# Kernel optimization log

Measured on AMD Instinct MI355X. Metric: run time of the kernel, lower is better.

## Reference

```python
import jax, jax.numpy as jnp
import numpy as np

N = 100000   # nodes
E = 1600000  # edges
R = 20       # relations
B = 8        # bases
F_IN = 32
H = 32
F_OUT = 32


def _rel_layer(x, src, dst, etypes, V, a, w_loop, bias, activation=None):
    """DGL RelGraphConv with basis decomposition, sum aggregation, self-loop, bias.

    message m_e = x[src_e] @ W_{r_e}, W_r = sum_b a[r,b] V[b]; h_v = sum_{e->v} m_e
    Since messages are linear in x, aggregate x[src] per (dst, rel) segment first,
    then apply the relation weights once per node: same math, far less traffic.
    """
    W = jnp.einsum('rb,bio->rio', a, V)                       # [R, in, out]
    seg = dst.astype(jnp.int32) * R + etypes.astype(jnp.int32)  # [E]
    agg = jax.ops.segment_sum(x[src], seg, num_segments=N * R)  # [N*R, in]
    agg = agg.reshape(N, R, -1)
    h = jnp.einsum('nri,rio->no', agg, W) + x @ w_loop + bias   # [N, out]
    if activation is not None:
        h = activation(h)
    return h


def setup_inputs() -> dict:
    key = jax.random.key(0)
    ks = jax.random.split(key, 10)
    s = 1.0 / np.sqrt(F_IN)
    return {
        'x': jax.random.normal(ks[0], (N, F_IN), dtype=jnp.float32),
        'src': jax.random.randint(ks[1], (E,), 0, N, dtype=jnp.int32),
        'dst': jax.random.randint(ks[2], (E,), 0, N, dtype=jnp.int32),
        'etypes': jax.random.randint(ks[3], (E,), 0, R, dtype=jnp.int32),
        'V1': jax.random.normal(ks[4], (B, F_IN, H), dtype=jnp.float32) * s,
        'a1': jax.random.normal(ks[5], (R, B), dtype=jnp.float32) * s,
        'loop1': jax.random.normal(ks[6], (F_IN, H), dtype=jnp.float32) * s,
        'b1': jnp.zeros((H,), dtype=jnp.float32),
        'V2': jax.random.normal(ks[7], (B, H, F_OUT), dtype=jnp.float32) * s,
        'a2': jax.random.normal(ks[8], (R, B), dtype=jnp.float32) * s,
        'loop2': jax.random.normal(ks[9], (H, F_OUT), dtype=jnp.float32) * s,
        'b2': jnp.zeros((F_OUT,), dtype=jnp.float32),
    }


def reference(x, src, dst, etypes, V1, a1, loop1, b1, V2, a2, loop2, b2):
    h = _rel_layer(x, src, dst, etypes, V1, a1, loop1, b1, activation=jax.nn.relu)
    h = _rel_layer(h, src, dst, etypes, V2, a2, loop2, b2, activation=None)
    return h
```

## Files before the change

### kernel.cpp

```cpp
#include <hip/hip_runtime.h>
#include <hip/hip_bf16.h>

#define NN 100000
#define NE 1600000
#define NR 20
#define NB 8
#define FD 32

#define EPB 8192
#define NBB ((NE + EPB - 1) / EPB)
#define NBKT ((NN + 255) / 256)

typedef short short8 __attribute__((ext_vector_type(8)));
typedef float f32x4  __attribute__((ext_vector_type(4)));

__device__ __forceinline__ unsigned short f2bf(float f) {
  union { float f; unsigned u; } c; c.f = f;
  unsigned r = c.u + 0x7FFF + ((c.u >> 16) & 1);
  return (unsigned short)(r >> 16);
}
__device__ __forceinline__ float bf2f(unsigned short u) {
  union { unsigned u; float f; } c; c.u = ((unsigned)u) << 16; return c.f;
}

__global__ void k_hist(const int* __restrict__ dst, int* __restrict__ hist) {
  int e = blockIdx.x * 256 + threadIdx.x;
  if (e < NE) atomicAdd(&hist[dst[e]], 1);
}

__global__ void k_scan1(int* __restrict__ data, int* __restrict__ aux, int n) {
  __shared__ int sd[256];
  int t = threadIdx.x, blk = blockIdx.x;
  int base = blk * 1024 + t * 4;
  int v[4];
#pragma unroll
  for (int j = 0; j < 4; ++j) v[j] = (base + j < n) ? data[base + j] : 0;
  int s = v[0] + v[1] + v[2] + v[3];
  sd[t] = s;
  __syncthreads();
  for (int off = 1; off < 256; off <<= 1) {
    int x = (t >= off) ? sd[t - off] : 0;
    __syncthreads();
    sd[t] += x;
    __syncthreads();
  }
  int run = sd[t] - s;
  if (t == 255) aux[blk] = sd[255];
#pragma unroll
  for (int j = 0; j < 4; ++j) {
    if (base + j < n) { data[base + j] = run; run += v[j]; }
  }
}

__global__ void k_scan2(int* __restrict__ aux, int n) {
  __shared__ int sd[256];
  int t = threadIdx.x;
  int loc[9];
  int s = 0;
#pragma unroll
  for (int j = 0; j < 9; ++j) {
    int idx = t * 9 + j;
    int v = (idx < n) ? aux[idx] : 0;
    loc[j] = s;
    s += v;
  }
  sd[t] = s;
  __syncthreads();
  for (int off = 1; off < 256; off <<= 1) {
    int x = (t >= off) ? sd[t - off] : 0;
    __syncthreads();
    sd[t] += x;
    __syncthreads();
  }
  int excl = sd[t] - s;
#pragma unroll
  for (int j = 0; j < 9; ++j) {
    int idx = t * 9 + j;
    if (idx < n) aux[idx] = excl + loc[j];
  }
}

__global__ void k_scan3(int* __restrict__ data, const int* __restrict__ aux, int n) {
  int i = blockIdx.x * 256 + threadIdx.x;
  if (i < n) data[i] += aux[i >> 10];
}

__global__ void k_endcap(int* __restrict__ ioffs) {
  if (threadIdx.x == 0 && blockIdx.x == 0) ioffs[NN] = NE;
}

__global__ void __launch_bounds__(256) k_bin(const int* __restrict__ src,
                                             const int* __restrict__ dst,
                                             const int* __restrict__ et,
                                             int* __restrict__ binbuf,
                                             int* __restrict__ bcnt,
                                             int* __restrict__ segoff) {
  __shared__ int sA[512], sB[512];
  int g = blockIdx.x, t = threadIdx.x;
  int e0 = g * EPB;
  int e1 = e0 + EPB; if (e1 > NE) e1 = NE;
  sA[t] = 0; sA[t + 256] = 0;
  __syncthreads();
  for (int e = e0 + t; e < e1; e += 256) atomicAdd(&sA[dst[e] >> 8], 1);
  __syncthreads();
  for (int b = t; b < NBKT; b += 256) bcnt[g * NBKT + b] = sA[b];
  int* pa = sA; int* pb = sB;
  for (int off = 1; off < 512; off <<= 1) {
    __syncthreads();
    for (int idx = t; idx < 512; idx += 256) {
      int v = pa[idx];
      if (idx >= off) v += pa[idx - off];
      pb[idx] = v;
    }
    int* tmp = pa; pa = pb; pb = tmp;
  }
  __syncthreads();
  for (int b = t; b < NBKT; b += 256) {
    int ex = b ? pa[b - 1] : 0;
    segoff[g * NBKT + b] = e0 + ex;
    pb[b] = ex;
  }
  __syncthreads();
  for (int e = e0 + t; e < e1; e += 256) {
    int d = dst[e];
    int pos = atomicAdd(&pb[d >> 8], 1);
    binbuf[e0 + pos] = (src[e] << 13) | ((d & 255) << 5) | et[e];
  }
}

__global__ void __launch_bounds__(256) k_bsort(const int* __restrict__ binbuf,
                                               const int* __restrict__ bcnt,
                                               const int* __restrict__ segoff,
                                               const int* __restrict__ ioffs,
                                               int* __restrict__ es) {
  __shared__ int cur[256];
  __shared__ int scnt[NBB], ssof[NBB];
  int b = blockIdx.x, t = threadIdx.x;
  int node = b * 256 + t;
  cur[t] = (node < NN) ? ioffs[node] : 0;
  for (int g = t; g < NBB; g += 256) {
    scnt[g] = bcnt[g * NBKT + b];
    ssof[g] = segoff[g * NBKT + b];
  }
  __syncthreads();
  int w = t >> 6, l = t & 63;
  for (int g = w; g < NBB; g += 4) {
    int c = scnt[g], so = ssof[g];
    for (int base = l; base < c; base += 64) {
      int v = binbuf[so + base];
      int j = (v >> 5) & 255;
      int pos = atomicAdd(&cur[j], 1);
      es[pos] = ((v >> 13) << 5) | (v & 31);
    }
  }
}

__global__ void k_xcast(const float* __restrict__ x, unsigned short* __restrict__ xb) {
  int t = blockIdx.x * 256 + threadIdx.x;
  if (t >= (NN * FD) / 8) return;
  const float4* xp = reinterpret_cast<const float4*>(x) + t * 2;
  float4 a = xp[0], b = xp[1];
  short8 v;
  v[0] = (short)f2bf(a.x); v[1] = (short)f2bf(a.y);
  v[2] = (short)f2bf(a.z); v[3] = (short)f2bf(a.w);
  v[4] = (short)f2bf(b.x); v[5] = (short)f2bf(b.y);
  v[6] = (short)f2bf(b.z); v[7] = (short)f2bf(b.w);
  reinterpret_cast<short8*>(xb)[t] = v;
}

__global__ void k_bfrag(const float* __restrict__ V1, const float* __restrict__ lp1,
                        const float* __restrict__ V2, const float* __restrict__ lp2,
                        unsigned short* __restrict__ Bf1, unsigned short* __restrict__ Bf2) {
  int t = blockIdx.x * 256 + threadIdx.x;
  if (t >= 2 * 9216) return;
  int layer = t / 9216;
  int idx = t - layer * 9216;
  int kstep = idx >> 10;
  int rem = idx & 1023;
  int otile = rem >> 9;
  int li = (rem >> 3) & 63;
  int j = idx & 7;
  int k = kstep * 32 + ((li >> 4) << 3) + j;
  int o = otile * 16 + (li & 15);
  const float* V = layer ? V2 : V1;
  const float* lp = layer ? lp2 : lp1;
  float val = (k < 256) ? V[k * 32 + o] : lp[(k - 256) * 32 + o];
  (layer ? Bf2 : Bf1)[idx] = f2bf(val);
}

__global__ void __launch_bounds__(256) k_edge(const unsigned short* __restrict__ xin,
                                              const int* __restrict__ ioffs,
                                              const int* __restrict__ es,
                                              const float* __restrict__ arel,
                                              unsigned short* __restrict__ zb,
                                              int n0, int n1) {
  int wid = (blockIdx.x * 256 + threadIdx.x) >> 6;
  int nw  = (gridDim.x * 256) >> 6;
  int l = threadIdx.x & 63;
  int i = l & 31, hh = l >> 5;
  const float4* aT = reinterpret_cast<const float4*>(arel);
  for (int v = n0 + wid; v < n1; v += nw) {
    int e0 = __builtin_amdgcn_readfirstlane(ioffs[v]);
    int e1 = __builtin_amdgcn_readfirstlane(ioffs[v + 1]);
    float z0 = 0.f, z1 = 0.f, z2 = 0.f, z3 = 0.f;
    int e = e0;
    for (; e + 8 <= e1; e += 8) {
      int r0 = es[e],     r1 = es[e + 1], r2 = es[e + 2], r3 = es[e + 3];
      int r4 = es[e + 4], r5 = es[e + 5], r6 = es[e + 6], r7 = es[e + 7];
      float x0 = bf2f(xin[((r0 >> 5) << 5) | i]);
      float x1 = bf2f(xin[((r1 >> 5) << 5) | i]);
      float x2 = bf2f(xin[((r2 >> 5) << 5) | i]);
      float x3 = bf2f(xin[((r3 >> 5) << 5) | i]);
      float x4 = bf2f(xin[((r4 >> 5) << 5) | i]);
      float x5 = bf2f(xin[((r5 >> 5) << 5) | i]);
      float x6 = bf2f(xin[((r6 >> 5) << 5) | i]);
      float x7 = bf2f(xin[((r7 >> 5) << 5) | i]);
      float4 a0 = aT[((r0 & 31) << 1) | hh];
      float4 a1 = aT[((r1 & 31) << 1) | hh];
      float4 a2 = aT[((r2 & 31) << 1) | hh];
      float4 a3 = aT[((r3 & 31) << 1) | hh];
      float4 a4 = aT[((r4 & 31) << 1) | hh];
      float4 a5 = aT[((r5 & 31) << 1) | hh];
      float4 a6 = aT[((r6 & 31) << 1) | hh];
      float4 a7 = aT[((r7 & 31) << 1) | hh];
      z0 += a0.x * x0; z1 += a0.y * x0; z2 += a0.z * x0; z3 += a0.w * x0;
      z0 += a1.x * x1; z1 += a1.y * x1; z2 += a1.z * x1; z3 += a1.w * x1;
      z0 += a2.x * x2; z1 += a2.y * x2; z2 += a2.z * x2; z3 += a2.w * x2;
      z0 += a3.x * x3; z1 += a3.y * x3; z2 += a3.z * x3; z3 += a3.w * x3;
      z0 += a4.x * x4; z1 += a4.y * x4; z2 += a4.z * x4; z3 += a4.w * x4;
      z0 += a5.x * x5; z1 += a5.y * x5; z2 += a5.z * x5; z3 += a5.w * x5;
      z0 += a6.x * x6; z1 += a6.y * x6; z2 += a6.z * x6; z3 += a6.w * x6;
      z0 += a7.x * x7; z1 += a7.y * x7; z2 += a7.z * x7; z3 += a7.w * x7;
    }
    for (; e + 4 <= e1; e += 4) {
      int r0 = es[e], r1 = es[e + 1], r2 = es[e + 2], r3 = es[e + 3];
      float x0 = bf2f(xin[((r0 >> 5) << 5) | i]);
      float x1 = bf2f(xin[((r1 >> 5) << 5) | i]);
      float x2 = bf2f(xin[((r2 >> 5) << 5) | i]);
      float x3 = bf2f(xin[((r3 >> 5) << 5) | i]);
      float4 a0 = aT[((r0 & 31) << 1) | hh];
      float4 a1 = aT[((r1 & 31) << 1) | hh];
      float4 a2 = aT[((r2 & 31) << 1) | hh];
      float4 a3 = aT[((r3 & 31) << 1) | hh];
      z0 += a0.x * x0; z1 += a0.y * x0; z2 += a0.z * x0; z3 += a0.w * x0;
      z0 += a1.x * x1; z1 += a1.y * x1; z2 += a1.z * x1; z3 += a1.w * x1;
      z0 += a2.x * x2; z1 += a2.y * x2; z2 += a2.z * x2; z3 += a2.w * x2;
      z0 += a3.x * x3; z1 += a3.y * x3; z2 += a3.z * x3; z3 += a3.w * x3;
    }
    for (; e < e1; ++e) {
      int rec = es[e];
      float xv = bf2f(xin[((rec >> 5) << 5) | i]);
      float4 av = aT[((rec & 31) << 1) | hh];
      z0 += av.x * xv; z1 += av.y * xv; z2 += av.z * xv; z3 += av.w * xv;
    }
    unsigned short* zp = zb + ((size_t)(v - n0) << 8) + (hh << 7) + i;
    zp[0]  = f2bf(z0);
    zp[32] = f2bf(z1);
    zp[64] = f2bf(z2);
    zp[96] = f2bf(z3);
  }
}

__global__ void __launch_bounds__(256) k_finish(const unsigned short* __restrict__ zb,
                                                const unsigned short* __restrict__ xin,
                                                const unsigned short* __restrict__ Bfrag,
                                                const float* __restrict__ bias,
                                                float* __restrict__ out_f32,
                                                unsigned short* __restrict__ out_bf16,
                                                int n0, int n1, int do_relu) {
  int lane = threadIdx.x & 63;
  int wid = (blockIdx.x * 256 + threadIdx.x) >> 6;
  int nwv = (gridDim.x * 256) >> 6;
  const short8* Bp = reinterpret_cast<const short8*>(Bfrag);
  short8 bf[9][2];
#pragma unroll
  for (int ks = 0; ks < 9; ++ks)
#pragma unroll
    for (int ot = 0; ot < 2; ++ot)
      bf[ks][ot] = Bp[((ks * 2 + ot) << 6) + lane];
  float bsv0 = bias[lane & 15];
  float bsv1 = bias[16 + (lane & 15)];
  int cnt = n1 - n0;
  int tiles = (cnt + 15) >> 4;
  int row = lane & 15;
  int kg = lane >> 4;
  for (int t = wid; t < tiles; t += nwv) {
    int nb = t << 4;
    int r = nb + row;
    int rc = (r < cnt) ? r : (cnt - 1);
    const short8* zrow = reinterpret_cast<const short8*>(zb + ((size_t)rc << 8));
    f32x4 acc0 = {0.f, 0.f, 0.f, 0.f};
    f32x4 acc1 = {0.f, 0.f, 0.f, 0.f};
#pragma unroll
    for (int ks = 0; ks < 8; ++ks) {
      short8 af = zrow[(ks << 2) + kg];
      acc0 = __builtin_amdgcn_mfma_f32_16x16x32_bf16(af, bf[ks][0], acc0, 0, 0, 0);
      acc1 = __builtin_amdgcn_mfma_f32_16x16x32_bf16(af, bf[ks][1], acc1, 0, 0, 0);
    }
    {
      short8 xs = *reinterpret_cast<const short8*>(xin + ((size_t)(n0 + rc) << 5) + (kg << 3));
      acc0 = __builtin_amdgcn_mfma_f32_16x16x32_bf16(xs, bf[8][0], acc0, 0, 0, 0);
      acc1 = __builtin_amdgcn_mfma_f32_16x16x32_bf16(xs, bf[8][1], acc1, 0, 0, 0);
    }
#pragma unroll
    for (int q = 0; q < 4; ++q) {
      int orow = (kg << 2) + q;
      int n = nb + orow;
      if (n < cnt) {
        float v0 = acc0[q] + bsv0;
        float v1 = acc1[q] + bsv1;
        if (do_relu) { v0 = fmaxf(v0, 0.f); v1 = fmaxf(v1, 0.f); }
        size_t base = ((size_t)(n0 + n) << 5);
        if (out_f32) { out_f32[base + row] = v0; out_f32[base + 16 + row] = v1; }
        if (out_bf16) { out_bf16[base + row] = f2bf(v0); out_bf16[base + 16 + row] = f2bf(v1); }
      }
    }
  }
}

extern "C" void kernel_launch(void* const* d_in, const int* in_sizes, int n_in,
                              void* d_out, int out_size, void* d_ws, size_t ws_size,
                              hipStream_t stream) {
  const float* x   = (const float*)d_in[0];
  const int* src   = (const int*)d_in[1];
  const int* dst   = (const int*)d_in[2];
  const int* et    = (const int*)d_in[3];
  const float* V1  = (const float*)d_in[4];
  const float* a1  = (const float*)d_in[5];
  const float* lp1 = (const float*)d_in[6];
  const float* b1  = (const float*)d_in[7];
  const float* V2  = (const float*)d_in[8];
  const float* a2  = (const float*)d_in[9];
  const float* lp2 = (const float*)d_in[10];
  const float* b2  = (const float*)d_in[11];
  float* out = (float*)d_out;

  char* w = (char*)d_ws;
  int* ioffs = (int*)(w + 0);
  int* aux   = (int*)(w + 400128);
  int* es    = (int*)(w + 400640);
  int* binbuf= (int*)(w + 6800640);
  int* bcnt  = (int*)(w + 13223168);
  int* segoff= (int*)(w + 13529728);
  unsigned short* xb  = (unsigned short*)(w + 13836288);
  unsigned short* h1b = (unsigned short*)(w + 20236288);
  unsigned short* Bf1 = (unsigned short*)(w + 26636288);
  unsigned short* Bf2 = (unsigned short*)(w + 26654720);
  const size_t ZB_OFF = 26673152;
  if (ws_size < ZB_OFF + (size_t)4096 * 512) return;
  unsigned short* zb = (unsigned short*)(w + ZB_OFF);
  int cap = (int)((ws_size - ZB_OFF) / 512);
  if (cap > NN) cap = NN;
  int nch = (NN + cap - 1) / cap;
  int cs  = (((NN + nch - 1) / nch) + 15) & ~15;

  hipMemsetAsync(ioffs, 0, (size_t)NN * 4, stream);

  k_hist<<<(NE + 255) / 256, 256, 0, stream>>>(dst, ioffs);

  int nScanBlk = (NN + 1023) / 1024;
  k_scan1<<<nScanBlk, 256, 0, stream>>>(ioffs, aux, NN);
  k_scan2<<<1, 256, 0, stream>>>(aux, nScanBlk);
  k_scan3<<<(NN + 255) / 256, 256, 0, stream>>>(ioffs, aux, NN);
  k_endcap<<<1, 64, 0, stream>>>(ioffs);

  k_bin<<<NBB, 256, 0, stream>>>(src, dst, et, binbuf, bcnt, segoff);
  k_bsort<<<NBKT, 256, 0, stream>>>(binbuf, bcnt, segoff, ioffs, es);

  k_xcast<<<((NN * FD / 8) + 255) / 256, 256, 0, stream>>>(x, xb);
  k_bfrag<<<(2 * 9216 + 255) / 256, 256, 0, stream>>>(V1, lp1, V2, lp2, Bf1, Bf2);

  for (int c = 0; c < nch; ++c) {
    int n0 = c * cs, n1 = n0 + cs;
    if (n1 > NN) n1 = NN;
    if (n0 >= n1) break;
    int tiles = ((n1 - n0) + 15) >> 4;
    int fblk = (tiles + 3) / 4; if (fblk > 512) fblk = 512;
    k_edge<<<2048, 256, 0, stream>>>(xb, ioffs, es, a1, zb, n0, n1);
    k_finish<<<fblk, 256, 0, stream>>>(zb, xb, Bf1, b1, nullptr, h1b, n0, n1, 1);
  }
  for (int c = 0; c < nch; ++c) {
    int n0 = c * cs, n1 = n0 + cs;
    if (n1 > NN) n1 = NN;
    if (n0 >= n1) break;
    int tiles = ((n1 - n0) + 15) >> 4;
    int fblk = (tiles + 3) / 4; if (fblk > 512) fblk = 512;
    k_edge<<<2048, 256, 0, stream>>>(h1b, ioffs, es, a2, zb, n0, n1);
    k_finish<<<fblk, 256, 0, stream>>>(zb, h1b, Bf2, b2, out, nullptr, n0, n1, 0);
  }
}
```

Measured before the change: 423.4 us.

## Fuse edge aggregation and MFMA finish into one per-layer kernel via LDS

Merges the per-node edge gather kernel and the MFMA projection kernel into a single k_layer kernel. Each wave aggregates 16 nodes, processing two nodes at a time to raise memory-level parallelism. It stores the bf16 basis-projected sums in swizzled LDS and runs the MFMA directly from LDS, so the zb round trip through global memory and the chunking loop go away. It also folds the endcap into k_bin and merges the xcast/bfrag prep kernels to cut launches. The trade-offs are 32KB of LDS per block, which limits occupancy, and fixed static work per wave in place of the previous grid-stride load balancing.

```diff
diff --git a/kernel.cpp b/kernel.cpp
--- a/kernel.cpp
+++ b/kernel.cpp
@@ -85,18 +85,16 @@
   if (i < n) data[i] += aux[i >> 10];
 }
 
-__global__ void k_endcap(int* __restrict__ ioffs) {
-  if (threadIdx.x == 0 && blockIdx.x == 0) ioffs[NN] = NE;
-}
-
 __global__ void __launch_bounds__(256) k_bin(const int* __restrict__ src,
                                              const int* __restrict__ dst,
                                              const int* __restrict__ et,
                                              int* __restrict__ binbuf,
                                              int* __restrict__ bcnt,
-                                             int* __restrict__ segoff) {
+                                             int* __restrict__ segoff,
+                                             int* __restrict__ ioffs) {
   __shared__ int sA[512], sB[512];
   int g = blockIdx.x, t = threadIdx.x;
+  if (g == 0 && t == 0) ioffs[NN] = NE;
   int e0 = g * EPB;
   int e1 = e0 + EPB; if (e1 > NE) e1 = NE;
   sA[t] = 0; sA[t + 256] = 0;
@@ -155,164 +153,192 @@
   }
 }
 
-__global__ void k_xcast(const float* __restrict__ x, unsigned short* __restrict__ xb) {
+__global__ void k_prep(const float* __restrict__ x, unsigned short* __restrict__ xb,
+                       const float* __restrict__ V1, const float* __restrict__ lp1,
+                       const float* __restrict__ V2, const float* __restrict__ lp2,
+                       unsigned short* __restrict__ Bf1, unsigned short* __restrict__ Bf2) {
   int t = blockIdx.x * 256 + threadIdx.x;
-  if (t >= (NN * FD) / 8) return;
-  const float4* xp = reinterpret_cast<const float4*>(x) + t * 2;
-  float4 a = xp[0], b = xp[1];
-  short8 v;
-  v[0] = (short)f2bf(a.x); v[1] = (short)f2bf(a.y);
-  v[2] = (short)f2bf(a.z); v[3] = (short)f2bf(a.w);
-  v[4] = (short)f2bf(b.x); v[5] = (short)f2bf(b.y);
-  v[6] = (short)f2bf(b.z); v[7] = (short)f2bf(b.w);
-  reinterpret_cast<short8*>(xb)[t] = v;
-}
-
-__global__ void k_bfrag(const float* __restrict__ V1, const float* __restrict__ lp1,
-                        const float* __restrict__ V2, const float* __restrict__ lp2,
-                        unsigned short* __restrict__ Bf1, unsigned short* __restrict__ Bf2) {
-  int t = blockIdx.x * 256 + threadIdx.x;
-  if (t >= 2 * 9216) return;
-  int layer = t / 9216;
-  int idx = t - layer * 9216;
-  int kstep = idx >> 10;
-  int rem = idx & 1023;
-  int otile = rem >> 9;
-  int li = (rem >> 3) & 63;
-  int j = idx & 7;
-  int k = kstep * 32 + ((li >> 4) << 3) + j;
-  int o = otile * 16 + (li & 15);
-  const float* V = layer ? V2 : V1;
-  const float* lp = layer ? lp2 : lp1;
-  float val = (k < 256) ? V[k * 32 + o] : lp[(k - 256) * 32 + o];
-  (layer ? Bf2 : Bf1)[idx] = f2bf(val);
-}
-
-__global__ void __launch_bounds__(256) k_edge(const unsigned short* __restrict__ xin,
-                                              const int* __restrict__ ioffs,
-                                              const int* __restrict__ es,
-                                              const float* __restrict__ arel,
-                                              unsigned short* __restrict__ zb,
-                                              int n0, int n1) {
-  int wid = (blockIdx.x * 256 + threadIdx.x) >> 6;
-  int nw  = (gridDim.x * 256) >> 6;
-  int l = threadIdx.x & 63;
+  if (t < (NN * FD) / 8) {
+    const float4* xp = reinterpret_cast<const float4*>(x) + t * 2;
+    float4 a = xp[0], b = xp[1];
+    short8 v;
+    v[0] = (short)f2bf(a.x); v[1] = (short)f2bf(a.y);
+    v[2] = (short)f2bf(a.z); v[3] = (short)f2bf(a.w);
+    v[4] = (short)f2bf(b.x); v[5] = (short)f2bf(b.y);
+    v[6] = (short)f2bf(b.z); v[7] = (short)f2bf(b.w);
+    reinterpret_cast<short8*>(xb)[t] = v;
+  }
+  if (t < 2 * 9216) {
+    int layer = t / 9216;
+    int idx = t - layer * 9216;
+    int kstep = idx >> 10;
+    int rem = idx & 1023;
+    int otile = rem >> 9;
+    int li = (rem >> 3) & 63;
+    int j = idx & 7;
+    int k = kstep * 32 + ((li >> 4) << 3) + j;
+    int o = otile * 16 + (li & 15);
+    const float* V = layer ? V2 : V1;
+    const float* lp = layer ? lp2 : lp1;
+    float val = (k < 256) ? V[k * 32 + o] : lp[(k - 256) * 32 + o];
+    (layer ? Bf2 : Bf1)[idx] = f2bf(val);
+  }
+}
+
+__global__ void __launch_bounds__(256) k_layer(
+    const unsigned short* __restrict__ xin,
+    const int* __restrict__ ioffs,
+    const int* __restrict__ es,
+    const float* __restrict__ arel,
+    const unsigned short* __restrict__ Bfrag,
+    const float* __restrict__ bias,
+    float* __restrict__ out_f32,
+    unsigned short* __restrict__ out_b16,
+    int do_relu) {
+  __shared__ __align__(16) unsigned short zl[64 * 256];
+  int t = threadIdx.x;
+  int w = t >> 6, l = t & 63;
   int i = l & 31, hh = l >> 5;
+  int nb = blockIdx.x * 64 + w * 16;
   const float4* aT = reinterpret_cast<const float4*>(arel);
-  for (int v = n0 + wid; v < n1; v += nw) {
-    int e0 = __builtin_amdgcn_readfirstlane(ioffs[v]);
-    int e1 = __builtin_amdgcn_readfirstlane(ioffs[v + 1]);
-    float z0 = 0.f, z1 = 0.f, z2 = 0.f, z3 = 0.f;
-    int e = e0;
-    for (; e + 8 <= e1; e += 8) {
-      int r0 = es[e],     r1 = es[e + 1], r2 = es[e + 2], r3 = es[e + 3];
-      int r4 = es[e + 4], r5 = es[e + 5], r6 = es[e + 6], r7 = es[e + 7];
-      float x0 = bf2f(xin[((r0 >> 5) << 5) | i]);
-      float x1 = bf2f(xin[((r1 >> 5) << 5) | i]);
-      float x2 = bf2f(xin[((r2 >> 5) << 5) | i]);
-      float x3 = bf2f(xin[((r3 >> 5) << 5) | i]);
-      float x4 = bf2f(xin[((r4 >> 5) << 5) | i]);
-      float x5 = bf2f(xin[((r5 >> 5) << 5) | i]);
-      float x6 = bf2f(xin[((r6 >> 5) << 5) | i]);
-      float x7 = bf2f(xin[((r7 >> 5) << 5) | i]);
-      float4 a0 = aT[((r0 & 31) << 1) | hh];
-      float4 a1 = aT[((r1 & 31) << 1) | hh];
-      float4 a2 = aT[((r2 & 31) << 1) | hh];
-      float4 a3 = aT[((r3 & 31) << 1) | hh];
-      float4 a4 = aT[((r4 & 31) << 1) | hh];
-      float4 a5 = aT[((r5 & 31) << 1) | hh];
-      float4 a6 = aT[((r6 & 31) << 1) | hh];
-      float4 a7 = aT[((r7 & 31) << 1) | hh];
-      z0 += a0.x * x0; z1 += a0.y * x0; z2 += a0.z * x0; z3 += a0.w * x0;
-      z0 += a1.x * x1; z1 += a1.y * x1; z2 += a1.z * x1; z3 += a1.w * x1;
-      z0 += a2.x * x2; z1 += a2.y * x2; z2 += a2.z * x2; z3 += a2.w * x2;
-      z0 += a3.x * x3; z1 += a3.y * x3; z2 += a3.z * x3; z3 += a3.w * x3;
-      z0 += a4.x * x4; z1 += a4.y * x4; z2 += a4.z * x4; z3 += a4.w * x4;
-      z0 += a5.x * x5; z1 += a5.y * x5; z2 += a5.z * x5; z3 += a5.w * x5;
-      z0 += a6.x * x6; z1 += a6.y * x6; z2 += a6.z * x6; z3 += a6.w * x6;
-      z0 += a7.x * x7; z1 += a7.y * x7; z2 += a7.z * x7; z3 += a7.w * x7;
-    }
-    for (; e + 4 <= e1; e += 4) {
-      int r0 = es[e], r1 = es[e + 1], r2 = es[e + 2], r3 = es[e + 3];
-      float x0 = bf2f(xin[((r0 >> 5) << 5) | i]);
-      float x1 = bf2f(xin[((r1 >> 5) << 5) | i]);
-      float x2 = bf2f(xin[((r2 >> 5) << 5) | i]);
-      float x3 = bf2f(xin[((r3 >> 5) << 5) | i]);
-      float4 a0 = aT[((r0 & 31) << 1) | hh];
-      float4 a1 = aT[((r1 & 31) << 1) | hh];
-      float4 a2 = aT[((r2 & 31) << 1) | hh];
-      float4 a3 = aT[((r3 & 31) << 1) | hh];
-      z0 += a0.x * x0; z1 += a0.y * x0; z2 += a0.z * x0; z3 += a0.w * x0;
-      z0 += a1.x * x1; z1 += a1.y * x1; z2 += a1.z * x1; z3 += a1.w * x1;
-      z0 += a2.x * x2; z1 += a2.y * x2; z2 += a2.z * x2; z3 += a2.w * x2;
-      z0 += a3.x * x3; z1 += a3.y * x3; z2 += a3.z * x3; z3 += a3.w * x3;
-    }
-    for (; e < e1; ++e) {
-      int rec = es[e];
+  unsigned short* zw = zl + (w << 12);
+
+  for (int p = 0; p < 8; ++p) {
+    int vA = nb + 2 * p, vB = vA + 1;
+    int eA = 0, eA1 = 0, eB = 0, eB1 = 0;
+    if (vA < NN) { eA = ioffs[vA]; eA1 = ioffs[vA + 1]; }
+    if (vB < NN) { eB = ioffs[vB]; eB1 = ioffs[vB + 1]; }
+    eA  = __builtin_amdgcn_readfirstlane(eA);
+    eA1 = __builtin_amdgcn_readfirstlane(eA1);
+    eB  = __builtin_amdgcn_readfirstlane(eB);
+    eB1 = __builtin_amdgcn_readfirstlane(eB1);
+    float zA0 = 0.f, zA1 = 0.f, zA2 = 0.f, zA3 = 0.f;
+    float zB0 = 0.f, zB1 = 0.f, zB2 = 0.f, zB3 = 0.f;
+    while ((eA + 4 <= eA1) & (eB + 4 <= eB1)) {
+      int a0 = es[eA], a1 = es[eA + 1], a2 = es[eA + 2], a3 = es[eA + 3];
+      int b0 = es[eB], b1 = es[eB + 1], b2 = es[eB + 2], b3 = es[eB + 3];
+      float xa0 = bf2f(xin[((a0 >> 5) << 5) | i]);
+      float xa1 = bf2f(xin[((a1 >> 5) << 5) | i]);
+      float xa2 = bf2f(xin[((a2 >> 5) << 5) | i]);
+      float xa3 = bf2f(xin[((a3 >> 5) << 5) | i]);
+      float xb0 = bf2f(xin[((b0 >> 5) << 5) | i]);
+      float xb1 = bf2f(xin[((b1 >> 5) << 5) | i]);
+      float xb2 = bf2f(xin[((b2 >> 5) << 5) | i]);
+      float xb3 = bf2f(xin[((b3 >> 5) << 5) | i]);
+      float4 ca0 = aT[((a0 & 31) << 1) | hh];
+      float4 ca1 = aT[((a1 & 31) << 1) | hh];
+      float4 ca2 = aT[((a2 & 31) << 1) | hh];
+      float4 ca3 = aT[((a3 & 31) << 1) | hh];
+      float4 cb0 = aT[((b0 & 31) << 1) | hh];
+      float4 cb1 = aT[((b1 & 31) << 1) | hh];
+      float4 cb2 = aT[((b2 & 31) << 1) | hh];
+      float4 cb3 = aT[((b3 & 31) << 1) | hh];
+      zA0 += ca0.x * xa0; zA1 += ca0.y * xa0; zA2 += ca0.z * xa0; zA3 += ca0.w * xa0;
+      zB0 += cb0.x * xb0; zB1 += cb0.y * xb0; zB2 += cb0.z * xb0; zB3 += cb0.w * xb0;
+      zA0 += ca1.x * xa1; zA1 += ca1.y * xa1; zA2 += ca1.z * xa1; zA3 += ca1.w * xa1;
+      zB0 += cb1.x * xb1; zB1 += cb1.y * xb1; zB2 += cb1.z * xb1; zB3 += cb1.w * xb1;
+      zA0 += ca2.x * xa2; zA1 += ca2.y * xa2; zA2 += ca2.z * xa2; zA3 += ca2.w * xa2;
+      zB0 += cb2.x * xb2; zB1 += cb2.y * xb2; zB2 += cb2.z * xb2; zB3 += cb2.w * xb2;
+      zA0 += ca3.x * xa3; zA1 += ca3.y * xa3; zA2 += ca3.z * xa3; zA3 += ca3.w * xa3;
+      zB0 += cb3.x * xb3; zB1 += cb3.y * xb3; zB2 += cb3.z * xb3; zB3 += cb3.w * xb3;
+      eA += 4; eB += 4;
+    }
+    while (eA + 4 <= eA1) {
+      int a0 = es[eA], a1 = es[eA + 1], a2 = es[eA + 2], a3 = es[eA + 3];
+      float xa0 = bf2f(xin[((a0 >> 5) << 5) | i]);
+      float xa1 = bf2f(xin[((a1 >> 5) << 5) | i]);
+      float xa2 = bf2f(xin[((a2 >> 5) << 5) | i]);
+      float xa3 = bf2f(xin[((a3 >> 5) << 5) | i]);
+      float4 ca0 = aT[((a0 & 31) << 1) | hh];
+      float4 ca1 = aT[((a1 & 31) << 1) | hh];
+      float4 ca2 = aT[((a2 & 31) << 1) | hh];
+      float4 ca3 = aT[((a3 & 31) << 1) | hh];
+      zA0 += ca0.x * xa0; zA1 += ca0.y * xa0; zA2 += ca0.z * xa0; zA3 += ca0.w * xa0;
+      zA0 += ca1.x * xa1; zA1 += ca1.y * xa1; zA2 += ca1.z * xa1; zA3 += ca1.w * xa1;
+      zA0 += ca2.x * xa2; zA1 += ca2.y * xa2; zA2 += ca2.z * xa2; zA3 += ca2.w * xa2;
+      zA0 += ca3.x * xa3; zA1 += ca3.y * xa3; zA2 += ca3.z * xa3; zA3 += ca3.w * xa3;
+      eA += 4;
+    }
+    while (eB + 4 <= eB1) {
+      int b0 = es[eB], b1 = es[eB + 1], b2 = es[eB + 2], b3 = es[eB + 3];
+      float xb0 = bf2f(xin[((b0 >> 5) << 5) | i]);
+      float xb1 = bf2f(xin[((b1 >> 5) << 5) | i]);
+      float xb2 = bf2f(xin[((b2 >> 5) << 5) | i]);
+      float xb3 = bf2f(xin[((b3 >> 5) << 5) | i]);
+      float4 cb0 = aT[((b0 & 31) << 1) | hh];
+      float4 cb1 = aT[((b1 & 31) << 1) | hh];
+      float4 cb2 = aT[((b2 & 31) << 1) | hh];
+      float4 cb3 = aT[((b3 & 31) << 1) | hh];
+      zB0 += cb0.x * xb0; zB1 += cb0.y * xb0; zB2 += cb0.z * xb0; zB3 += cb0.w * xb0;
+      zB0 += cb1.x * xb1; zB1 += cb1.y * xb1; zB2 += cb1.z * xb1; zB3 += cb1.w * xb1;
+      zB0 += cb2.x * xb2; zB1 += cb2.y * xb2; zB2 += cb2.z * xb2; zB3 += cb2.w * xb2;
+      zB0 += cb3.x * xb3; zB1 += cb3.y * xb3; zB2 += cb3.z * xb3; zB3 += cb3.w * xb3;
+      eB += 4;
+    }
+    for (; eA < eA1; ++eA) {
+      int rec = es[eA];
       float xv = bf2f(xin[((rec >> 5) << 5) | i]);
       float4 av = aT[((rec & 31) << 1) | hh];
-      z0 += av.x * xv; z1 += av.y * xv; z2 += av.z * xv; z3 += av.w * xv;
-    }
-    unsigned short* zp = zb + ((size_t)(v - n0) << 8) + (hh << 7) + i;
-    zp[0]  = f2bf(z0);
-    zp[32] = f2bf(z1);
-    zp[64] = f2bf(z2);
-    zp[96] = f2bf(z3);
-  }
-}
-
-__global__ void __launch_bounds__(256) k_finish(const unsigned short* __restrict__ zb,
-                                                const unsigned short* __restrict__ xin,
-                                                const unsigned short* __restrict__ Bfrag,
-                                                const float* __restrict__ bias,
-                                                float* __restrict__ out_f32,
-                                                unsigned short* __restrict__ out_bf16,
-                                                int n0, int n1, int do_relu) {
-  int lane = threadIdx.x & 63;
-  int wid = (blockIdx.x * 256 + threadIdx.x) >> 6;
-  int nwv = (gridDim.x * 256) >> 6;
+      zA0 += av.x * xv; zA1 += av.y * xv; zA2 += av.z * xv; zA3 += av.w * xv;
+    }
+    for (; eB < eB1; ++eB) {
+      int rec = es[eB];
+      float xv = bf2f(xin[((rec >> 5) << 5) | i]);
+      float4 av = aT[((rec & 31) << 1) | hh];
+      zB0 += av.x * xv; zB1 += av.y * xv; zB2 += av.z * xv; zB3 += av.w * xv;
+    }
+    {
+      int r = 2 * p;
+      char* base = (char*)zw + (r << 9);
+      int sw = (r & 7) << 4;
+      int off = (hh << 8) | (i << 1);
+      *(unsigned short*)(base + ((off      ) ^ sw)) = f2bf(zA0);
+      *(unsigned short*)(base + ((off +  64) ^ sw)) = f2bf(zA1);
+      *(unsigned short*)(base + ((off + 128) ^ sw)) = f2bf(zA2);
+      *(unsigned short*)(base + ((off + 192) ^ sw)) = f2bf(zA3);
+    }
+    {
+      int r = 2 * p + 1;
+      char* base = (char*)zw + (r << 9);
+      int sw = (r & 7) << 4;
+      int off = (hh << 8) | (i << 1);
+      *(unsigned short*)(base + ((off      ) ^ sw)) = f2bf(zB0);
+      *(unsigned short*)(base + ((off +  64) ^ sw)) = f2bf(zB1);
+      *(unsigned short*)(base + ((off + 128) ^ sw)) = f2bf(zB2);
+      *(unsigned short*)(base + ((off + 192) ^ sw)) = f2bf(zB3);
+    }
+  }
+
+  int row = l & 15, kg = l >> 4;
+  short8 af[9];
+  {
+    char* rb = (char*)zw + (row << 9);
+    int sw = (row & 7) << 4;
+#pragma unroll
+    for (int ks = 0; ks < 8; ++ks)
+      af[ks] = *(const short8*)(rb + (((ks << 6) | (kg << 4)) ^ sw));
+    int nA = nb + row;
+    int nAc = (nA < NN) ? nA : (NN - 1);
+    af[8] = *(const short8*)(xin + ((size_t)nAc << 5) + (kg << 3));
+  }
   const short8* Bp = reinterpret_cast<const short8*>(Bfrag);
-  short8 bf[9][2];
-#pragma unroll
-  for (int ks = 0; ks < 9; ++ks)
-#pragma unroll
-    for (int ot = 0; ot < 2; ++ot)
-      bf[ks][ot] = Bp[((ks * 2 + ot) << 6) + lane];
-  float bsv0 = bias[lane & 15];
-  float bsv1 = bias[16 + (lane & 15)];
-  int cnt = n1 - n0;
-  int tiles = (cnt + 15) >> 4;
-  int row = lane & 15;
-  int kg = lane >> 4;
-  for (int t = wid; t < tiles; t += nwv) {
-    int nb = t << 4;
-    int r = nb + row;
-    int rc = (r < cnt) ? r : (cnt - 1);
-    const short8* zrow = reinterpret_cast<const short8*>(zb + ((size_t)rc << 8));
-    f32x4 acc0 = {0.f, 0.f, 0.f, 0.f};
-    f32x4 acc1 = {0.f, 0.f, 0.f, 0.f};
-#pragma unroll
-    for (int ks = 0; ks < 8; ++ks) {
-      short8 af = zrow[(ks << 2) + kg];
-      acc0 = __builtin_amdgcn_mfma_f32_16x16x32_bf16(af, bf[ks][0], acc0, 0, 0, 0);
-      acc1 = __builtin_amdgcn_mfma_f32_16x16x32_bf16(af, bf[ks][1], acc1, 0, 0, 0);
-    }
-    {
-      short8 xs = *reinterpret_cast<const short8*>(xin + ((size_t)(n0 + rc) << 5) + (kg << 3));
-      acc0 = __builtin_amdgcn_mfma_f32_16x16x32_bf16(xs, bf[8][0], acc0, 0, 0, 0);
-      acc1 = __builtin_amdgcn_mfma_f32_16x16x32_bf16(xs, bf[8][1], acc1, 0, 0, 0);
-    }
+  for (int ot = 0; ot < 2; ++ot) {
+    f32x4 acc = {0.f, 0.f, 0.f, 0.f};
+#pragma unroll
+    for (int ks = 0; ks < 9; ++ks) {
+      short8 bfv = Bp[((ks * 2 + ot) << 6) + l];
+      acc = __builtin_amdgcn_mfma_f32_16x16x32_bf16(af[ks], bfv, acc, 0, 0, 0);
+    }
+    float bs = bias[(ot << 4) + row];
 #pragma unroll
     for (int q = 0; q < 4; ++q) {
-      int orow = (kg << 2) + q;
-      int n = nb + orow;
-      if (n < cnt) {
-        float v0 = acc0[q] + bsv0;
-        float v1 = acc1[q] + bsv1;
-        if (do_relu) { v0 = fmaxf(v0, 0.f); v1 = fmaxf(v1, 0.f); }
-        size_t base = ((size_t)(n0 + n) << 5);
-        if (out_f32) { out_f32[base + row] = v0; out_f32[base + 16 + row] = v1; }
-        if (out_bf16) { out_bf16[base + row] = f2bf(v0); out_bf16[base + 16 + row] = f2bf(v1); }
+      int n = nb + (kg << 2) + q;
+      if (n < NN) {
+        float v = acc[q] + bs;
+        if (do_relu) v = fmaxf(v, 0.f);
+        size_t idx = ((size_t)n << 5) + (ot << 4) + row;
+        if (out_f32) out_f32[idx] = v;
+        else         out_b16[idx] = f2bf(v);
       }
     }
   }
@@ -336,23 +362,17 @@
   float* out = (float*)d_out;
 
   char* w = (char*)d_ws;
-  int* ioffs = (int*)(w + 0);
-  int* aux   = (int*)(w + 400128);
-  int* es    = (int*)(w + 400640);
-  int* binbuf= (int*)(w + 6800640);
-  int* bcnt  = (int*)(w + 13223168);
-  int* segoff= (int*)(w + 13529728);
+  int* ioffs  = (int*)(w + 0);
+  int* aux    = (int*)(w + 400128);
+  int* es     = (int*)(w + 400640);
+  int* binbuf = (int*)(w + 6800640);
+  int* bcnt   = (int*)(w + 13223168);
+  int* segoff = (int*)(w + 13529728);
   unsigned short* xb  = (unsigned short*)(w + 13836288);
   unsigned short* h1b = (unsigned short*)(w + 20236288);
   unsigned short* Bf1 = (unsigned short*)(w + 26636288);
   unsigned short* Bf2 = (unsigned short*)(w + 26654720);
-  const size_t ZB_OFF = 26673152;
-  if (ws_size < ZB_OFF + (size_t)4096 * 512) return;
-  unsigned short* zb = (unsigned short*)(w + ZB_OFF);
-  int cap = (int)((ws_size - ZB_OFF) / 512);
-  if (cap > NN) cap = NN;
-  int nch = (NN + cap - 1) / cap;
-  int cs  = (((NN + nch - 1) / nch) + 15) & ~15;
+  if (ws_size < 26673152) return;
 
   hipMemsetAsync(ioffs, 0, (size_t)NN * 4, stream);
 
@@ -362,30 +382,13 @@
   k_scan1<<<nScanBlk, 256, 0, stream>>>(ioffs, aux, NN);
   k_scan2<<<1, 256, 0, stream>>>(aux, nScanBlk);
   k_scan3<<<(NN + 255) / 256, 256, 0, stream>>>(ioffs, aux, NN);
-  k_endcap<<<1, 64, 0, stream>>>(ioffs);
-
-  k_bin<<<NBB, 256, 0, stream>>>(src, dst, et, binbuf, bcnt, segoff);
+
+  k_bin<<<NBB, 256, 0, stream>>>(src, dst, et, binbuf, bcnt, segoff, ioffs);
   k_bsort<<<NBKT, 256, 0, stream>>>(binbuf, bcnt, segoff, ioffs, es);
 
-  k_xcast<<<((NN * FD / 8) + 255) / 256, 256, 0, stream>>>(x, xb);
-  k_bfrag<<<(2 * 9216 + 255) / 256, 256, 0, stream>>>(V1, lp1, V2, lp2, Bf1, Bf2);
-
-  for (int c = 0; c < nch; ++c) {
-    int n0 = c * cs, n1 = n0 + cs;
-    if (n1 > NN) n1 = NN;
-    if (n0 >= n1) break;
-    int tiles = ((n1 - n0) + 15) >> 4;
-    int fblk = (tiles + 3) / 4; if (fblk > 512) fblk = 512;
-    k_edge<<<2048, 256, 0, stream>>>(xb, ioffs, es, a1, zb, n0, n1);
-    k_finish<<<fblk, 256, 0, stream>>>(zb, xb, Bf1, b1, nullptr, h1b, n0, n1, 1);
-  }
-  for (int c = 0; c < nch; ++c) {
-    int n0 = c * cs, n1 = n0 + cs;
-    if (n1 > NN) n1 = NN;
-    if (n0 >= n1) break;
-    int tiles = ((n1 - n0) + 15) >> 4;
-    int fblk = (tiles + 3) / 4; if (fblk > 512) fblk = 512;
-    k_edge<<<2048, 256, 0, stream>>>(h1b, ioffs, es, a2, zb, n0, n1);
-    k_finish<<<fblk, 256, 0, stream>>>(zb, h1b, Bf2, b2, out, nullptr, n0, n1, 0);
-  }
-}
+  k_prep<<<(((NN * FD) / 8) + 255) / 256, 256, 0, stream>>>(x, xb, V1, lp1, V2, lp2, Bf1, Bf2);
+
+  int nblk = (NN + 63) / 64;
+  k_layer<<<nblk, 256, 0, stream>>>(xb, ioffs, es, a1, Bf1, b1, nullptr, h1b, 1);
+  k_layer<<<nblk, 256, 0, stream>>>(h1b, ioffs, es, a2, Bf2, b2, out, nullptr, 0);
+}
```

Result: faster. 398.1 us (-6.0%).
